# Performance work log

Measured on AMD Instinct MI355X. Metric: run time of the kernel, lower is better.

The kernel has to match this reference:

```python
import jax, jax.numpy as jnp
import numpy as np


def setup_inputs() -> dict:
    key = jax.random.key(0)
    k1, k2, k3 = jax.random.split(key, 3)
    B, S, D, H = 16, 4096, 512, 512
    inp = jax.random.normal(k1, (B, S, D), dtype=jnp.float32)
    # torch nn.Linear(D, 3*H): weight (3H, D), bias (3H,)
    W = jax.random.normal(k2, (3 * H, D), dtype=jnp.float32) * (1.0 / np.sqrt(D))
    b = jax.random.normal(k3, (3 * H,), dtype=jnp.float32) * 0.01
    return {"inp": inp, "W": W, "b": b}


def _forget_mult(z, f):
    # z, f: (B, S, H). h_t = f_t*z_t + (1-f_t)*h_{t-1}, h_{-1}=0 (hid=None)
    zt = jnp.swapaxes(z, 0, 1)  # (S, B, H)
    ft = jnp.swapaxes(f, 0, 1)
    h0 = jnp.zeros(z.shape[0:1] + z.shape[2:3], dtype=z.dtype)  # (B, H)

    def step(h, zf):
        zi, fi = zf
        h = fi * zi + (1.0 - fi) * h
        return h, h

    _, hs = jax.lax.scan(step, h0, (zt, ft))
    return jnp.swapaxes(hs, 0, 1)  # (B, S, H)


def reference(inp, W, b):
    # QRNNLayer forward: window=1, output_gate=True, batch_first=True,
    # backward=False, zoneout=0, hid=None.
    y = jnp.einsum('bsd,hd->bsh', inp, W) + b  # (B, S, 3H)
    z_gate, f_gate, o_gate = jnp.split(y, 3, axis=2)
    z_gate = jnp.tanh(z_gate)
    f_gate = jax.nn.sigmoid(f_gate)
    c_gate = _forget_mult(z_gate, f_gate)
    output = jax.nn.sigmoid(o_gate) * c_gate
    return output, c_gate[:, -1]
```

## Files before the change

kernel.cpp:

```cpp
#include <hip/hip_runtime.h>
#include <stdint.h>

#define Bdim 16
#define Sdim 4096
#define Hdim 512
#define Mdim (Bdim*Sdim)
#define N3   (3*Hdim)
#define Kdim 512
#define NCHUNK 64
#define CLEN  (Sdim/NCHUNK)

typedef __bf16 bf16;
typedef __bf16 bf16x4 __attribute__((ext_vector_type(4)));
typedef __bf16 bf16x8 __attribute__((ext_vector_type(8)));
typedef float  f32x4  __attribute__((ext_vector_type(4)));
typedef _Float16 f16;
typedef _Float16 f16x4 __attribute__((ext_vector_type(4)));
typedef _Float16 f16x8 __attribute__((ext_vector_type(8)));

__device__ inline void gload_lds16(const void* g, void* l) {
  __builtin_amdgcn_global_load_lds(
      (const __attribute__((address_space(1))) uint32_t*)g,
      (__attribute__((address_space(3))) uint32_t*)l, 16, 0, 0);
}

__global__ void __launch_bounds__(256) cvt_kernel(const float4* __restrict__ in,
                                                  bf16x4* __restrict__ out, int n4) {
  int i = blockIdx.x * blockDim.x + threadIdx.x;
  if (i >= n4) return;
  float4 v = in[i];
  bf16x4 o;
  o.x = (bf16)v.x; o.y = (bf16)v.y; o.z = (bf16)v.z; o.w = (bf16)v.w;
  out[i] = o;
}

#define BM 256
#define BN 256
#define BK 64
#define NIT (Kdim/BK)

__global__ void __launch_bounds__(512, 2) gemm_act_kernel(
    const bf16* __restrict__ A, const bf16* __restrict__ Wb,
    const float* __restrict__ bias,
    f16* __restrict__ zbuf, f16* __restrict__ fbuf, f16* __restrict__ ogbuf) {
  __shared__ char lds[131072];
  const int tid  = threadIdx.x;
  const int wid  = tid >> 6;
  const int lane = tid & 63;
  const int wr = wid >> 2, wc = wid & 3;
  const int bid = blockIdx.x;
  const int wg  = (bid & 7) * 192 + (bid >> 3);
  const int mt = wg / (N3 / BN);
  const int nt = wg % (N3 / BN);
  const int row0 = mt * BM, col0 = nt * BN;

  const bf16* Ag = A  + (size_t)row0 * Kdim;
  const bf16* Bg = Wb + (size_t)col0 * Kdim;

  uint32_t srcOff[4], dstB[4];
  #pragma unroll
  for (int i = 0; i < 4; ++i) {
    int c = i * 512 + tid;
    int r = c >> 3, slot = c & 7;
    srcOff[i] = (uint32_t)(r * Kdim + ((slot ^ (r & 7)) << 3));
    dstB[i]   = (uint32_t)((i * 512 + wid * 64) * 16);
  }
  uint32_t aOff[8], bOff[4];
  #pragma unroll
  for (int m = 0; m < 8; ++m) {
    int row = wr * 128 + m * 16 + (lane & 15);
    aOff[m] = (uint32_t)((row * 128 + (lane >> 4) * 16) ^ ((row & 7) << 4));
  }
  #pragma unroll
  for (int n = 0; n < 4; ++n) {
    int row = wc * 64 + n * 16 + (lane & 15);
    bOff[n] = (uint32_t)((row * 128 + (lane >> 4) * 16) ^ ((row & 7) << 4));
  }

  f32x4 acc[8][4];
  #pragma unroll
  for (int m = 0; m < 8; ++m)
    #pragma unroll
    for (int n = 0; n < 4; ++n)
      acc[m][n] = (f32x4){0.f, 0.f, 0.f, 0.f};

  {
    char* Ad = lds; char* Bd = lds + 32768;
    #pragma unroll
    for (int i = 0; i < 4; ++i) gload_lds16(Ag + srcOff[i], Ad + dstB[i]);
    #pragma unroll
    for (int i = 0; i < 4; ++i) gload_lds16(Bg + srcOff[i], Bd + dstB[i]);
  }
  __syncthreads();

  for (int t = 0; t < NIT; ++t) {
    if (t + 1 < NIT) {
      int k0 = (t + 1) * BK;
      char* Ad = lds + ((t + 1) & 1) * 65536; char* Bd = Ad + 32768;
      #pragma unroll
      for (int i = 0; i < 4; ++i) gload_lds16(Ag + srcOff[i] + k0, Ad + dstB[i]);
      #pragma unroll
      for (int i = 0; i < 4; ++i) gload_lds16(Bg + srcOff[i] + k0, Bd + dstB[i]);
    }
    const char* Ab = lds + (t & 1) * 65536;
    const char* Bb = Ab + 32768;
    #pragma unroll
    for (int kk = 0; kk < 2; ++kk) {
      bf16x8 af[8], bf[4];
      #pragma unroll
      for (int m = 0; m < 8; ++m) af[m] = *(const bf16x8*)(Ab + (aOff[m] ^ (kk << 6)));
      #pragma unroll
      for (int n = 0; n < 4; ++n) bf[n] = *(const bf16x8*)(Bb + (bOff[n] ^ (kk << 6)));
      #pragma unroll
      for (int m = 0; m < 8; ++m)
        #pragma unroll
        for (int n = 0; n < 4; ++n)
          acc[m][n] = __builtin_amdgcn_mfma_f32_16x16x32_bf16(af[m], bf[n], acc[m][n], 0, 0, 0);
    }
    __syncthreads();
  }

  const int gate = nt >> 1;
  const int cb   = (nt & 1) * 256;
  f16* dst = (gate == 0) ? zbuf : ((gate == 1) ? fbuf : ogbuf);
  float bv[4];
  #pragma unroll
  for (int n = 0; n < 4; ++n)
    bv[n] = bias[gate * Hdim + cb + wc * 64 + n * 16 + (lane & 15)];

  #pragma unroll
  for (int m = 0; m < 8; ++m) {
    #pragma unroll
    for (int n = 0; n < 4; ++n) {
      int col = wc * 64 + n * 16 + (lane & 15);
      #pragma unroll
      for (int r = 0; r < 4; ++r) {
        int row = wr * 128 + m * 16 + (lane >> 4) * 4 + r;
        float y = acc[m][n][r] + bv[n];
        float v;
        if (gate == 0) {
          float e = __expf(2.f * y);
          v = 1.f - 2.f / (e + 1.f);
        } else {
          v = 1.f / (1.f + __expf(-y));
        }
        uint32_t byte = (uint32_t)(row * 512 + col * 2) ^ ((uint32_t)(row & 7) << 4);
        *(f16*)(lds + byte) = (f16)v;
      }
    }
  }
  __syncthreads();
  #pragma unroll
  for (int j = 0; j < 16; ++j) {
    int c = j * 512 + tid;
    int row = c >> 5, col8 = c & 31;
    uint32_t byte = (uint32_t)(row * 512 + col8 * 16) ^ ((uint32_t)(row & 7) << 4);
    f16x8 v = *(const f16x8*)(lds + byte);
    *(f16x8*)&dst[(size_t)(row0 + row) * Hdim + cb + col8 * 8] = v;
  }
}

__global__ void __launch_bounds__(256) scanA_kernel(const f16x4* __restrict__ z4,
                                                    const f16x4* __restrict__ f4,
                                                    float* __restrict__ Pb,
                                                    float* __restrict__ Qb) {
  int u  = blockIdx.x * blockDim.x + threadIdx.x;
  int hq = u & 127;
  int bc = u >> 7;
  int b  = bc & (Bdim - 1);
  int c  = bc >> 4;
  size_t base = ((size_t)(b * Sdim + c * CLEN)) * 128 + hq;
  float P[4] = {1.f, 1.f, 1.f, 1.f}, Q[4] = {0.f, 0.f, 0.f, 0.f};
  #pragma unroll 4
  for (int s = 0; s < CLEN; ++s) {
    f16x4 fv = f4[base], zv = z4[base];
    #pragma unroll
    for (int j = 0; j < 4; ++j) {
      float f = (float)fv[j];
      Q[j] += f * ((float)zv[j] - Q[j]);
      P[j] *= (1.f - f);
    }
    base += 128;
  }
  int outi = ((c * Bdim + b) << 9) + hq * 4;
  *(float4*)&Pb[outi] = make_float4(P[0], P[1], P[2], P[3]);
  *(float4*)&Qb[outi] = make_float4(Q[0], Q[1], Q[2], Q[3]);
}

__global__ void __launch_bounds__(256) scanB_kernel(const float* __restrict__ Pb,
                                                    const float* __restrict__ Qb,
                                                    float* __restrict__ hin,
                                                    float* __restrict__ c_last) {
  int t = blockIdx.x * blockDim.x + threadIdx.x;
  int h = t & (Hdim - 1), b = t >> 9;
  float hs = 0.f;
  #pragma unroll 8
  for (int c = 0; c < NCHUNK; ++c) {
    hin[c * (Bdim * Hdim) + t] = hs;
    int u = ((c * Bdim + b) << 9) + h;
    hs = Pb[u] * hs + Qb[u];
  }
  c_last[t] = hs;
}

__global__ void __launch_bounds__(256) scanC_kernel(const f16x4* __restrict__ z4,
                                                    const f16x4* __restrict__ f4,
                                                    const f16x4* __restrict__ og4,
                                                    const float* __restrict__ hin,
                                                    float4* __restrict__ out4) {
  int u  = blockIdx.x * blockDim.x + threadIdx.x;
  int hq = u & 127;
  int bc = u >> 7;
  int b  = bc & (Bdim - 1);
  int c  = bc >> 4;
  float4 hv = *(const float4*)&hin[c * (Bdim * Hdim) + b * Hdim + hq * 4];
  float h[4] = {hv.x, hv.y, hv.z, hv.w};
  size_t base = ((size_t)(b * Sdim + c * CLEN)) * 128 + hq;
  #pragma unroll 4
  for (int s = 0; s < CLEN; ++s) {
    f16x4 fv = f4[base], zv = z4[base], ov = og4[base];
    float4 o;
    #pragma unroll
    for (int j = 0; j < 4; ++j) {
      h[j] += (float)fv[j] * ((float)zv[j] - h[j]);
    }
    o.x = (float)ov[0] * h[0]; o.y = (float)ov[1] * h[1];
    o.z = (float)ov[2] * h[2]; o.w = (float)ov[3] * h[3];
    out4[base] = o;
    base += 128;
  }
}

extern "C" void kernel_launch(void* const* d_in, const int* in_sizes, int n_in,
                              void* d_out, int out_size, void* d_ws, size_t ws_size,
                              hipStream_t stream) {
  const float* inp  = (const float*)d_in[0];
  const float* W    = (const float*)d_in[1];
  const float* bias = (const float*)d_in[2];
  float* out = (float*)d_out;

  char* ws = (char*)d_ws;
  bf16* Abf = (bf16*)(ws);
  bf16* Wbf = (bf16*)(ws + 67108864);
  f16*  zh  = (f16*) (ws + 68681728);
  f16*  fh  = (f16*) (ws + 135790592);
  f16*  ogh = (f16*) (ws + 202899456);
  float* Pb = (float*)(ws + 270008320);
  float* Qb = (float*)(ws + 272105472);
  float* hin= (float*)(ws + 274202624);

  {
    int n4 = (Mdim * Kdim) / 4;
    cvt_kernel<<<n4 / 256, 256, 0, stream>>>((const float4*)inp, (bf16x4*)Abf, n4);
  }
  {
    int n4 = (N3 * Kdim) / 4;
    cvt_kernel<<<n4 / 256, 256, 0, stream>>>((const float4*)W, (bf16x4*)Wbf, n4);
  }
  gemm_act_kernel<<<(Mdim / BM) * (N3 / BN), 512, 0, stream>>>(Abf, Wbf, bias,
                                                               zh, fh, ogh);
  scanA_kernel<<<(NCHUNK * Bdim * 128) / 256, 256, 0, stream>>>(
      (const f16x4*)zh, (const f16x4*)fh, Pb, Qb);
  scanB_kernel<<<(Bdim * Hdim) / 256, 256, 0, stream>>>(Pb, Qb, hin,
                                                        out + (size_t)Mdim * Hdim);
  scanC_kernel<<<(NCHUNK * Bdim * 128) / 256, 256, 0, stream>>>(
      (const f16x4*)zh, (const f16x4*)fh, (const f16x4*)ogh, hin, (float4*)out);
}
```

Measured before the change: 310.7 us.

## Switch GEMM mainloop to 4-stage ring buffer with BK=32 and fine-grained waits

Replaces the double-buffered BK=64 mainloop with a four-slot LDS ring of BK=32 tiles, prefetching three stages ahead. Global loads are tracked with explicit vmcnt waits and raw s_barrier in place of full __syncthreads, so later loads stay in flight while MFMAs run. The swizzle is reworked for 64-byte rows and s_setprio raises the wave priority around the MFMA block. The aim is to hide global-load latency better; the cost is more barriers per K and hand-tuned wait counts that must match the number of loads in flight.

After: 312.7 us. About the same (+0.6%).

```diff
diff --git a/kernel.cpp b/kernel.cpp
--- a/kernel.cpp
+++ b/kernel.cpp
@@ -18,7 +18,7 @@
 typedef _Float16 f16x4 __attribute__((ext_vector_type(4)));
 typedef _Float16 f16x8 __attribute__((ext_vector_type(8)));
 
-__device__ inline void gload_lds16(const void* g, void* l) {
+__device__ __forceinline__ void gload_lds16(const void* g, void* l) {
   __builtin_amdgcn_global_load_lds(
       (const __attribute__((address_space(1))) uint32_t*)g,
       (__attribute__((address_space(3))) uint32_t*)l, 16, 0, 0);
@@ -36,8 +36,8 @@
 
 #define BM 256
 #define BN 256
-#define BK 64
-#define NIT (Kdim/BK)
+#define BK2 32
+#define NT (Kdim/BK2)
 
 __global__ void __launch_bounds__(512, 2) gemm_act_kernel(
     const bf16* __restrict__ A, const bf16* __restrict__ Wb,
@@ -52,29 +52,35 @@
   const int wg  = (bid & 7) * 192 + (bid >> 3);
   const int mt = wg / (N3 / BN);
   const int nt = wg % (N3 / BN);
-  const int row0 = mt * BM, col0 = nt * BN;
+  const int row0 = mt * BM;
 
   const bf16* Ag = A  + (size_t)row0 * Kdim;
-  const bf16* Bg = Wb + (size_t)col0 * Kdim;
-
-  uint32_t srcOff[4], dstB[4];
-  #pragma unroll
-  for (int i = 0; i < 4; ++i) {
-    int c = i * 512 + tid;
-    int r = c >> 3, slot = c & 7;
-    srcOff[i] = (uint32_t)(r * Kdim + ((slot ^ (r & 7)) << 3));
-    dstB[i]   = (uint32_t)((i * 512 + wid * 64) * 16);
-  }
-  uint32_t aOff[8], bOff[4];
-  #pragma unroll
-  for (int m = 0; m < 8; ++m) {
-    int row = wr * 128 + m * 16 + (lane & 15);
-    aOff[m] = (uint32_t)((row * 128 + (lane >> 4) * 16) ^ ((row & 7) << 4));
-  }
-  #pragma unroll
-  for (int n = 0; n < 4; ++n) {
-    int row = wc * 64 + n * 16 + (lane & 15);
-    bOff[n] = (uint32_t)((row * 128 + (lane >> 4) * 16) ^ ((row & 7) << 4));
+  const bf16* Bg = Wb + (size_t)(nt * BN) * Kdim;
+
+  uint32_t srcO[2];
+  {
+    int rlo = tid >> 2, spos = tid & 3;
+    #pragma unroll
+    for (int i = 0; i < 2; ++i) {
+      int row = i * 128 + rlo;
+      srcO[i] = (uint32_t)(row * Kdim + ((spos ^ ((row >> 1) & 3)) << 3));
+    }
+  }
+  const uint32_t dstBase = (uint32_t)(wid * 1024);
+
+  uint32_t byteA[8], byteB[4];
+  {
+    int kslot = lane >> 4;
+    #pragma unroll
+    for (int m = 0; m < 8; ++m) {
+      int row = wr * 128 + m * 16 + (lane & 15);
+      byteA[m] = (uint32_t)(row * 64 + ((kslot ^ ((row >> 1) & 3)) << 4));
+    }
+    #pragma unroll
+    for (int n = 0; n < 4; ++n) {
+      int row = wc * 64 + n * 16 + (lane & 15);
+      byteB[n] = (uint32_t)(16384 + row * 64 + ((kslot ^ ((row >> 1) & 3)) << 4));
+    }
   }
 
   f32x4 acc[8][4];
@@ -84,41 +90,58 @@
     for (int n = 0; n < 4; ++n)
       acc[m][n] = (f32x4){0.f, 0.f, 0.f, 0.f};
 
-  {
-    char* Ad = lds; char* Bd = lds + 32768;
-    #pragma unroll
-    for (int i = 0; i < 4; ++i) gload_lds16(Ag + srcOff[i], Ad + dstB[i]);
-    #pragma unroll
-    for (int i = 0; i < 4; ++i) gload_lds16(Bg + srcOff[i], Bd + dstB[i]);
-  }
+  #pragma unroll
+  for (int kt = 0; kt < 3; ++kt) {
+    char* ring = lds + kt * 32768;
+    #pragma unroll
+    for (int i = 0; i < 2; ++i)
+      gload_lds16(Ag + srcO[i] + kt * BK2, ring + i * 8192 + dstBase);
+    #pragma unroll
+    for (int i = 0; i < 2; ++i)
+      gload_lds16(Bg + srcO[i] + kt * BK2, ring + 16384 + i * 8192 + dstBase);
+  }
+  asm volatile("s_waitcnt vmcnt(8)" ::: "memory");
+  __builtin_amdgcn_s_barrier();
+  __builtin_amdgcn_sched_barrier(0);
+
+  #pragma unroll
+  for (int t = 0; t < NT; ++t) {
+    if (t + 3 < NT) {
+      char* ring = lds + ((t + 3) & 3) * 32768;
+      #pragma unroll
+      for (int i = 0; i < 2; ++i)
+        gload_lds16(Ag + srcO[i] + (t + 3) * BK2, ring + i * 8192 + dstBase);
+      #pragma unroll
+      for (int i = 0; i < 2; ++i)
+        gload_lds16(Bg + srcO[i] + (t + 3) * BK2, ring + 16384 + i * 8192 + dstBase);
+    }
+    const char* Ab = lds + (t & 3) * 32768;
+    bf16x8 af[8], bfrag[4];
+    #pragma unroll
+    for (int m = 0; m < 8; ++m) af[m] = *(const bf16x8*)(Ab + byteA[m]);
+    #pragma unroll
+    for (int n = 0; n < 4; ++n) bfrag[n] = *(const bf16x8*)(Ab + byteB[n]);
+    __builtin_amdgcn_s_setprio(1);
+    #pragma unroll
+    for (int m = 0; m < 8; ++m)
+      #pragma unroll
+      for (int n = 0; n < 4; ++n)
+        acc[m][n] = __builtin_amdgcn_mfma_f32_16x16x32_bf16(af[m], bfrag[n], acc[m][n], 0, 0, 0);
+    __builtin_amdgcn_s_setprio(0);
+    if (t <= NT - 4) {
+      asm volatile("s_waitcnt vmcnt(8)" ::: "memory");
+    } else if (t == NT - 3) {
+      asm volatile("s_waitcnt vmcnt(4)" ::: "memory");
+    } else if (t == NT - 2) {
+      asm volatile("s_waitcnt vmcnt(0)" ::: "memory");
+    }
+    if (t < NT - 1) {
+      __builtin_amdgcn_s_barrier();
+      __builtin_amdgcn_sched_barrier(0);
+    }
+  }
+
   __syncthreads();
-
-  for (int t = 0; t < NIT; ++t) {
-    if (t + 1 < NIT) {
-      int k0 = (t + 1) * BK;
-      char* Ad = lds + ((t + 1) & 1) * 65536; char* Bd = Ad + 32768;
-      #pragma unroll
-      for (int i = 0; i < 4; ++i) gload_lds16(Ag + srcOff[i] + k0, Ad + dstB[i]);
-      #pragma unroll
-      for (int i = 0; i < 4; ++i) gload_lds16(Bg + srcOff[i] + k0, Bd + dstB[i]);
-    }
-    const char* Ab = lds + (t & 1) * 65536;
-    const char* Bb = Ab + 32768;
-    #pragma unroll
-    for (int kk = 0; kk < 2; ++kk) {
-      bf16x8 af[8], bf[4];
-      #pragma unroll
-      for (int m = 0; m < 8; ++m) af[m] = *(const bf16x8*)(Ab + (aOff[m] ^ (kk << 6)));
-      #pragma unroll
-      for (int n = 0; n < 4; ++n) bf[n] = *(const bf16x8*)(Bb + (bOff[n] ^ (kk << 6)));
-      #pragma unroll
-      for (int m = 0; m < 8; ++m)
-        #pragma unroll
-        for (int n = 0; n < 4; ++n)
-          acc[m][n] = __builtin_amdgcn_mfma_f32_16x16x32_bf16(af[m], bf[n], acc[m][n], 0, 0, 0);
-    }
-    __syncthreads();
-  }
 
   const int gate = nt >> 1;
   const int cb   = (nt & 1) * 256;
```

## Software-pipeline GEMM main loop with quarter-tile staging and interleaved MFMA chunks

Applied to the files above, without the earlier changes.

Replaces the simple double-buffered K loop in the fused GEMM+activation kernel with a fully unrolled schedule. Each K tile is split into four 16-MFMA chunks, global-to-LDS loads are issued in half-tile pieces ahead of time, and explicit vmcnt/lgkmcnt waits with barriers and s_setprio interleave LDS reads, global loads and MFMAs. The goal is to hide load latency and keep the matrix units busy, in exchange for more barriers and careful hand-tuned wait counts that could break if they are wrong.

Result: no change. 308.4 us (-0.7%).

```diff
diff --git a/kernel.cpp b/kernel.cpp
--- a/kernel.cpp
+++ b/kernel.cpp
@@ -18,7 +18,7 @@
 typedef _Float16 f16x4 __attribute__((ext_vector_type(4)));
 typedef _Float16 f16x8 __attribute__((ext_vector_type(8)));
 
-__device__ inline void gload_lds16(const void* g, void* l) {
+__device__ __forceinline__ void gload_lds16(const void* g, void* l) {
   __builtin_amdgcn_global_load_lds(
       (const __attribute__((address_space(1))) uint32_t*)g,
       (__attribute__((address_space(3))) uint32_t*)l, 16, 0, 0);
@@ -36,8 +36,90 @@
 
 #define BM 256
 #define BN 256
-#define BK 64
-#define NIT (Kdim/BK)
+#define BKT 64
+#define NKT (Kdim/BKT)
+
+__device__ __forceinline__ bf16x8 lds_ld(const char* p) { return *(const bf16x8*)p; }
+
+__device__ __forceinline__ void read_af(bf16x8 (&d)[4][2], const char* Lb, uint32_t base,
+                                        uint32_t swk0, uint32_t swk1, int mh) {
+  #pragma unroll
+  for (int i = 0; i < 4; ++i) {
+    d[i][0] = lds_ld(Lb + base + mh * 8192 + i * 2048 + swk0);
+    d[i][1] = lds_ld(Lb + base + mh * 8192 + i * 2048 + swk1);
+  }
+}
+__device__ __forceinline__ void read_bf(bf16x8 (&d)[2][2], const char* Lb, uint32_t base,
+                                        uint32_t swk0, uint32_t swk1, int nh) {
+  #pragma unroll
+  for (int j = 0; j < 2; ++j) {
+    d[j][0] = lds_ld(Lb + base + nh * 4096 + j * 2048 + swk0);
+    d[j][1] = lds_ld(Lb + base + nh * 4096 + j * 2048 + swk1);
+  }
+}
+__device__ __forceinline__ void chunk16(f32x4 (&acc)[8][4], const bf16x8 (&a)[4][2],
+                                        const bf16x8 (&b)[2][2], int mb, int nb) {
+  __builtin_amdgcn_s_setprio(1);
+  #pragma unroll
+  for (int i = 0; i < 4; ++i)
+    #pragma unroll
+    for (int j = 0; j < 2; ++j)
+      #pragma unroll
+      for (int kk = 0; kk < 2; ++kk)
+        acc[mb + i][nb + j] =
+            __builtin_amdgcn_mfma_f32_16x16x32_bf16(a[i][kk], b[j][kk], acc[mb + i][nb + j], 0, 0, 0);
+  __builtin_amdgcn_s_setprio(0);
+}
+
+template <int H>
+__device__ __forceinline__ void stage_half(const bf16* Ag, const bf16* Bg, char* lds,
+                                           uint32_t so0, uint32_t wbase) {
+  if constexpr (H <= 4 * NKT - 1) {
+    constexpr int th = H >> 2, ss = H & 3;
+    constexpr uint32_t goff = (uint32_t)((ss >> 1) * 128 * Kdim + th * BKT);
+    constexpr uint32_t lbase = (uint32_t)((th & 1) * 65536 + (ss & 1) * 32768 + (ss >> 1) * 16384);
+    const bf16* gp = (ss & 1) ? Bg : Ag;
+    gload_lds16(gp + goff + so0,         lds + lbase + wbase);
+    gload_lds16(gp + goff + so0 + 32768, lds + lbase + 8192 + wbase);
+  }
+}
+
+#define BAR()   __builtin_amdgcn_s_barrier()
+#define LGKM0() do { asm volatile("s_waitcnt lgkmcnt(0)" ::: "memory"); \
+                     __builtin_amdgcn_sched_barrier(0); } while (0)
+
+template <int T>
+__device__ __forceinline__ void ktile(char* lds, f32x4 (&acc)[8][4],
+    bf16x8 (&af0)[4][2], bf16x8 (&af1)[4][2], bf16x8 (&bf0)[2][2], bf16x8 (&bf1)[2][2],
+    const bf16* Ag, const bf16* Bg, uint32_t so0, uint32_t wbase,
+    uint32_t aBase, uint32_t bBase, uint32_t swk0, uint32_t swk1) {
+  const char* Lb = lds + (T & 1) * 65536;
+  read_af(af0, Lb, aBase, swk0, swk1, 0);
+  read_bf(bf0, Lb, bBase, swk0, swk1, 0);
+  stage_half<4 * T + 6>(Ag, Bg, lds, so0, wbase);
+  BAR(); LGKM0();
+  chunk16(acc, af0, bf0, 0, 0);
+  BAR();
+  read_af(af1, Lb, aBase, swk0, swk1, 1);
+  stage_half<4 * T + 7>(Ag, Bg, lds, so0, wbase);
+  BAR(); LGKM0();
+  chunk16(acc, af1, bf0, 4, 0);
+  BAR();
+  read_bf(bf1, Lb, bBase, swk0, swk1, 1);
+  stage_half<4 * T + 8>(Ag, Bg, lds, so0, wbase);
+  BAR(); LGKM0();
+  chunk16(acc, af1, bf1, 4, 2);
+  BAR();
+  stage_half<4 * T + 9>(Ag, Bg, lds, so0, wbase);
+  BAR(); LGKM0();
+  chunk16(acc, af0, bf1, 0, 2);
+  if constexpr (T <= NKT - 3) {
+    asm volatile("s_waitcnt vmcnt(4)" ::: "memory");
+  } else if constexpr (T == NKT - 2) {
+    asm volatile("s_waitcnt vmcnt(0)" ::: "memory");
+  }
+  BAR();
+}
 
 __global__ void __launch_bounds__(512, 2) gemm_act_kernel(
     const bf16* __restrict__ A, const bf16* __restrict__ Wb,
@@ -52,30 +134,20 @@
   const int wg  = (bid & 7) * 192 + (bid >> 3);
   const int mt = wg / (N3 / BN);
   const int nt = wg % (N3 / BN);
-  const int row0 = mt * BM, col0 = nt * BN;
+  const int row0 = mt * BM;
 
   const bf16* Ag = A  + (size_t)row0 * Kdim;
-  const bf16* Bg = Wb + (size_t)col0 * Kdim;
-
-  uint32_t srcOff[4], dstB[4];
-  #pragma unroll
-  for (int i = 0; i < 4; ++i) {
-    int c = i * 512 + tid;
-    int r = c >> 3, slot = c & 7;
-    srcOff[i] = (uint32_t)(r * Kdim + ((slot ^ (r & 7)) << 3));
-    dstB[i]   = (uint32_t)((i * 512 + wid * 64) * 16);
-  }
-  uint32_t aOff[8], bOff[4];
-  #pragma unroll
-  for (int m = 0; m < 8; ++m) {
-    int row = wr * 128 + m * 16 + (lane & 15);
-    aOff[m] = (uint32_t)((row * 128 + (lane >> 4) * 16) ^ ((row & 7) << 4));
-  }
-  #pragma unroll
-  for (int n = 0; n < 4; ++n) {
-    int row = wc * 64 + n * 16 + (lane & 15);
-    bOff[n] = (uint32_t)((row * 128 + (lane >> 4) * 16) ^ ((row & 7) << 4));
-  }
+  const bf16* Bg = Wb + (size_t)(nt * BN) * Kdim;
+
+  const uint32_t r0   = tid >> 3;
+  const uint32_t slot = tid & 7;
+  const uint32_t so0  = r0 * Kdim + ((slot ^ (r0 & 7)) << 3);
+  const uint32_t wbase = (uint32_t)(wid * 1024);
+  const uint32_t kslot = lane >> 4;
+  const uint32_t swk0 = ((kslot)     ^ (uint32_t)(lane & 7)) << 4;
+  const uint32_t swk1 = ((4 + kslot) ^ (uint32_t)(lane & 7)) << 4;
+  const uint32_t aBase = (uint32_t)((wr * 128 + (lane & 15)) * 128);
+  const uint32_t bBase = (uint32_t)(32768 + (wc * 64 + (lane & 15)) * 128);
 
   f32x4 acc[8][4];
   #pragma unroll
@@ -83,42 +155,27 @@
     #pragma unroll
     for (int n = 0; n < 4; ++n)
       acc[m][n] = (f32x4){0.f, 0.f, 0.f, 0.f};
-
-  {
-    char* Ad = lds; char* Bd = lds + 32768;
-    #pragma unroll
-    for (int i = 0; i < 4; ++i) gload_lds16(Ag + srcOff[i], Ad + dstB[i]);
-    #pragma unroll
-    for (int i = 0; i < 4; ++i) gload_lds16(Bg + srcOff[i], Bd + dstB[i]);
-  }
+  bf16x8 af0[4][2], af1[4][2], bf0[2][2], bf1[2][2];
+
+  stage_half<0>(Ag, Bg, lds, so0, wbase);
+  stage_half<1>(Ag, Bg, lds, so0, wbase);
+  stage_half<2>(Ag, Bg, lds, so0, wbase);
+  stage_half<3>(Ag, Bg, lds, so0, wbase);
+  stage_half<4>(Ag, Bg, lds, so0, wbase);
+  stage_half<5>(Ag, Bg, lds, so0, wbase);
+  asm volatile("s_waitcnt vmcnt(4)" ::: "memory");
+  BAR();
+
+  ktile<0>(lds, acc, af0, af1, bf0, bf1, Ag, Bg, so0, wbase, aBase, bBase, swk0, swk1);
+  ktile<1>(lds, acc, af0, af1, bf0, bf1, Ag, Bg, so0, wbase, aBase, bBase, swk0, swk1);
+  ktile<2>(lds, acc, af0, af1, bf0, bf1, Ag, Bg, so0, wbase, aBase, bBase, swk0, swk1);
+  ktile<3>(lds, acc, af0, af1, bf0, bf1, Ag, Bg, so0, wbase, aBase, bBase, swk0, swk1);
+  ktile<4>(lds, acc, af0, af1, bf0, bf1, Ag, Bg, so0, wbase, aBase, bBase, swk0, swk1);
+  ktile<5>(lds, acc, af0, af1, bf0, bf1, Ag, Bg, so0, wbase, aBase, bBase, swk0, swk1);
+  ktile<6>(lds, acc, af0, af1, bf0, bf1, Ag, Bg, so0, wbase, aBase, bBase, swk0, swk1);
+  ktile<7>(lds, acc, af0, af1, bf0, bf1, Ag, Bg, so0, wbase, aBase, bBase, swk0, swk1);
+
   __syncthreads();
-
-  for (int t = 0; t < NIT; ++t) {
-    if (t + 1 < NIT) {
-      int k0 = (t + 1) * BK;
-      char* Ad = lds + ((t + 1) & 1) * 65536; char* Bd = Ad + 32768;
-      #pragma unroll
-      for (int i = 0; i < 4; ++i) gload_lds16(Ag + srcOff[i] + k0, Ad + dstB[i]);
-      #pragma unroll
-      for (int i = 0; i < 4; ++i) gload_lds16(Bg + srcOff[i] + k0, Bd + dstB[i]);
-    }
-    const char* Ab = lds + (t & 1) * 65536;
-    const char* Bb = Ab + 32768;
-    #pragma unroll
-    for (int kk = 0; kk < 2; ++kk) {
-      bf16x8 af[8], bf[4];
-      #pragma unroll
-      for (int m = 0; m < 8; ++m) af[m] = *(const bf16x8*)(Ab + (aOff[m] ^ (kk << 6)));
-      #pragma unroll
-      for (int n = 0; n < 4; ++n) bf[n] = *(const bf16x8*)(Bb + (bOff[n] ^ (kk << 6)));
-      #pragma unroll
-      for (int m = 0; m < 8; ++m)
-        #pragma unroll
-        for (int n = 0; n < 4; ++n)
-          acc[m][n] = __builtin_amdgcn_mfma_f32_16x16x32_bf16(af[m], bf[n], acc[m][n], 0, 0, 0);
-    }
-    __syncthreads();
-  }
 
   const int gate = nt >> 1;
   const int cb   = (nt & 1) * 256;
```
